# Kernel optimization log

Measured on AMD Instinct MI355X. Metric: run time of the kernel, lower is better.

The kernel has to match this reference:

```python
import jax, jax.numpy as jnp
import numpy as np

B, S, D, N = 8, 4096, 768, 64


def setup_inputs() -> dict:
    key = jax.random.key(0)
    k1, k2 = jax.random.split(key)
    word_vectors = jax.random.normal(k1, (B, S, D), dtype=jnp.float32)
    sent_rep_token_ids = jnp.sort(jax.random.randint(k2, (B, N), 0, S), axis=1)
    sent_rep_mask = jnp.ones((B, N), dtype=jnp.float32)
    # sent_lengths: each row must sum exactly to S (torch.split contract).
    rng = np.random.default_rng(0)
    lens = np.stack([
        np.diff(np.concatenate([[0], np.sort(rng.choice(np.arange(1, S), N - 1, replace=False)), [S]]))
        for _ in range(B)
    ])
    sent_lengths = jnp.asarray(lens, dtype=jnp.int64) if jax.config.jax_enable_x64 else jnp.asarray(lens, dtype=jnp.int32)
    sent_lengths_mask = jnp.ones((B, N), dtype=jnp.float32)
    return {
        "word_vectors": word_vectors,
        "sent_rep_token_ids": sent_rep_token_ids,
        "sent_rep_mask": sent_rep_mask,
        "sent_lengths": sent_lengths,
        "sent_lengths_mask": sent_lengths_mask,
    }


def reference(word_vectors, sent_rep_token_ids, sent_rep_mask, sent_lengths, sent_lengths_mask):
    b, s, d = word_vectors.shape
    n = sent_lengths.shape[1]
    dt = word_vectors.dtype

    # --- sent_rep_tokens branch: gather CLS-style token per sentence ---
    rep_vec = jnp.take_along_axis(word_vectors, sent_rep_token_ids[:, :, None], axis=1)  # [B,N,D]
    rep_vec = rep_vec * sent_rep_mask[:, :, None].astype(dt)

    # --- mean_tokens branch: ragged per-segment mean via segment_sum ---
    ends = jnp.cumsum(sent_lengths, axis=1)                      # [B,N] exclusive-end offsets
    pos = jnp.arange(s)
    seg = jax.vmap(lambda e: jnp.searchsorted(e, pos, side='right'))(ends)  # [B,S] segment id per token
    gseg = (seg + jnp.arange(b)[:, None] * n).reshape(-1)        # global segment ids [B*S]
    flat = word_vectors.reshape(b * s, d)
    sums = jax.ops.segment_sum(flat, gseg, num_segments=b * n).reshape(b, n, d)
    counts = jax.ops.segment_sum((flat != 0).astype(dt), gseg, num_segments=b * n).reshape(b, n, d)
    mean = sums / jnp.maximum(counts, 1)
    # fallback to word_vectors[0,0] when a segment has zero nonzero entries (original semantics)
    all_zero = (counts.sum(axis=-1) == 0)                        # [B,N]
    mean = jnp.where(all_zero[:, :, None], word_vectors[0, 0], mean)
    mean_vec = mean * sent_lengths_mask[:, :, None].astype(dt)

    out_vectors = jnp.concatenate([rep_vec, mean_vec], axis=1)   # [B,2N,D]
    out_masks = jnp.concatenate([sent_rep_mask, sent_lengths_mask], axis=1)  # [B,2N]
    return out_vectors, out_masks
```

## Files before the change

### kernel.cpp

```cpp
#include <hip/hip_runtime.h>

#define BB 8
#define SS 4096
#define DD 768
#define NN 64
#define D4 (DD / 4)

__global__ __launch_bounds__(64) void pool_kernel(
    const float* __restrict__ wv,
    const int* __restrict__ rep_ids,
    const float* __restrict__ rep_mask,
    const int* __restrict__ lens,
    const float* __restrict__ len_mask,
    float* __restrict__ out)
{
    const int seg  = blockIdx.x;
    const int g    = blockIdx.y;
    const int b    = seg >> 6;
    const int n    = seg & 63;
    const int lane = threadIdx.x;

    int myLen = lens[b * NN + lane];
    int pre   = (lane < n) ? myLen : 0;
    #pragma unroll
    for (int off = 32; off; off >>= 1) pre += __shfl_xor(pre, off);
    const int start = pre;
    const int len   = __shfl(myLen, n);

    const int col4 = g * 64 + lane;
    const float4* wv4 = (const float4*)wv;
    const float4* p   = wv4 + (size_t)(b * SS + start) * D4 + col4;

    float4 sum = make_float4(0.f, 0.f, 0.f, 0.f);
    float4 cnt = make_float4(0.f, 0.f, 0.f, 0.f);
    #pragma unroll 4
    for (int t = 0; t < len; ++t) {
        float4 v = p[(size_t)t * D4];
        sum.x += v.x; sum.y += v.y; sum.z += v.z; sum.w += v.w;
        cnt.x += (v.x != 0.f) ? 1.f : 0.f;
        cnt.y += (v.y != 0.f) ? 1.f : 0.f;
        cnt.z += (v.z != 0.f) ? 1.f : 0.f;
        cnt.w += (v.w != 0.f) ? 1.f : 0.f;
    }

    float4 mean;
    mean.x = sum.x / fmaxf(cnt.x, 1.f);
    mean.y = sum.y / fmaxf(cnt.y, 1.f);
    mean.z = sum.z / fmaxf(cnt.z, 1.f);
    mean.w = sum.w / fmaxf(cnt.w, 1.f);

    float tot = cnt.x + cnt.y + cnt.z + cnt.w;
    unsigned long long nz = __ballot(tot != 0.f);
    if (nz == 0ULL) {
        mean = wv4[col4];
    }

    const float lm = len_mask[b * NN + n];
    mean.x *= lm; mean.y *= lm; mean.z *= lm; mean.w *= lm;

    float4* out4 = (float4*)out;
    out4[(size_t)(b * 2 * NN + NN + n) * D4 + col4] = mean;

    const int   rid = rep_ids[b * NN + n];
    const float rm  = rep_mask[b * NN + n];
    float4 rv = wv4[(size_t)(b * SS + rid) * D4 + col4];
    rv.x *= rm; rv.y *= rm; rv.z *= rm; rv.w *= rm;
    out4[(size_t)(b * 2 * NN + n) * D4 + col4] = rv;

    if (g == 0 && lane == 0) {
        float* masks = out + (size_t)BB * 2 * NN * DD;
        masks[b * 2 * NN + n]      = rm;
        masks[b * 2 * NN + NN + n] = lm;
    }
}

extern "C" void kernel_launch(void* const* d_in, const int* in_sizes, int n_in,
                              void* d_out, int out_size, void* d_ws, size_t ws_size,
                              hipStream_t stream) {
    const float* wv       = (const float*)d_in[0];
    const int*   rep_ids  = (const int*)d_in[1];
    const float* rep_mask = (const float*)d_in[2];
    const int*   lens     = (const int*)d_in[3];
    const float* len_mask = (const float*)d_in[4];
    float*       out      = (float*)d_out;

    dim3 grid(BB * NN, 3);
    pool_kernel<<<grid, 64, 0, stream>>>(wv, rep_ids, rep_mask, lens, len_mask, out);
}
```

Baseline: 195.2 us.

## Split each segment's token loop across eight waves with shared-memory reduction

Each block now runs eight wavefronts. Each wave accumulates a strided subset of the segment's tokens, then wave 0 reduces the partial sums and counts held in LDS and writes the outputs. Before, a single wave walked the whole ragged segment serially, which gave only 1536 waves in flight and long per-wave dependency chains on a bandwidth-bound read of about 100 MB. The change adds a __syncthreads and an LDS reduction, and it leaves seven waves idle during the epilogue.

```diff
diff --git a/kernel.cpp b/kernel.cpp
--- a/kernel.cpp
+++ b/kernel.cpp
@@ -5,8 +5,10 @@
 #define DD 768
 #define NN 64
 #define D4 (DD / 4)
+#define WAVES 8
+#define BLOCK (WAVES * 64)
 
-__global__ __launch_bounds__(64) void pool_kernel(
+__global__ __launch_bounds__(BLOCK) void pool_kernel(
     const float* __restrict__ wv,
     const int* __restrict__ rep_ids,
     const float* __restrict__ rep_mask,
@@ -14,11 +16,16 @@
     const float* __restrict__ len_mask,
     float* __restrict__ out)
 {
+    __shared__ float4 s_sum[WAVES][64];
+    __shared__ float4 s_cnt[WAVES][64];
+
     const int seg  = blockIdx.x;
     const int g    = blockIdx.y;
     const int b    = seg >> 6;
     const int n    = seg & 63;
-    const int lane = threadIdx.x;
+    const int tid  = threadIdx.x;
+    const int lane = tid & 63;
+    const int w    = tid >> 6;
 
     int myLen = lens[b * NN + lane];
     int pre   = (lane < n) ? myLen : 0;
@@ -29,13 +36,14 @@
 
     const int col4 = g * 64 + lane;
     const float4* wv4 = (const float4*)wv;
-    const float4* p   = wv4 + (size_t)(b * SS + start) * D4 + col4;
+    const float4* p   = wv4 + ((size_t)(b * SS + start) + w) * D4 + col4;
 
     float4 sum = make_float4(0.f, 0.f, 0.f, 0.f);
     float4 cnt = make_float4(0.f, 0.f, 0.f, 0.f);
-    #pragma unroll 4
-    for (int t = 0; t < len; ++t) {
-        float4 v = p[(size_t)t * D4];
+    #pragma unroll 8
+    for (int t = w; t < len; t += WAVES) {
+        float4 v = *p;
+        p += (size_t)WAVES * D4;
         sum.x += v.x; sum.y += v.y; sum.z += v.z; sum.w += v.w;
         cnt.x += (v.x != 0.f) ? 1.f : 0.f;
         cnt.y += (v.y != 0.f) ? 1.f : 0.f;
@@ -43,34 +51,50 @@
         cnt.w += (v.w != 0.f) ? 1.f : 0.f;
     }
 
-    float4 mean;
-    mean.x = sum.x / fmaxf(cnt.x, 1.f);
-    mean.y = sum.y / fmaxf(cnt.y, 1.f);
-    mean.z = sum.z / fmaxf(cnt.z, 1.f);
-    mean.w = sum.w / fmaxf(cnt.w, 1.f);
+    s_sum[w][lane] = sum;
+    s_cnt[w][lane] = cnt;
+    __syncthreads();
 
-    float tot = cnt.x + cnt.y + cnt.z + cnt.w;
-    unsigned long long nz = __ballot(tot != 0.f);
-    if (nz == 0ULL) {
-        mean = wv4[col4];
-    }
+    if (w == 0) {
+        float4 S = make_float4(0.f, 0.f, 0.f, 0.f);
+        float4 C = make_float4(0.f, 0.f, 0.f, 0.f);
+        #pragma unroll
+        for (int j = 0; j < WAVES; ++j) {
+            float4 a = s_sum[j][lane];
+            float4 c = s_cnt[j][lane];
+            S.x += a.x; S.y += a.y; S.z += a.z; S.w += a.w;
+            C.x += c.x; C.y += c.y; C.z += c.z; C.w += c.w;
+        }
 
-    const float lm = len_mask[b * NN + n];
-    mean.x *= lm; mean.y *= lm; mean.z *= lm; mean.w *= lm;
+        float4 mean;
+        mean.x = S.x / fmaxf(C.x, 1.f);
+        mean.y = S.y / fmaxf(C.y, 1.f);
+        mean.z = S.z / fmaxf(C.z, 1.f);
+        mean.w = S.w / fmaxf(C.w, 1.f);
 
-    float4* out4 = (float4*)out;
-    out4[(size_t)(b * 2 * NN + NN + n) * D4 + col4] = mean;
+        float tot = C.x + C.y + C.z + C.w;
+        unsigned long long nz = __ballot(tot != 0.f);
+        if (nz == 0ULL) {
+            mean = wv4[col4];
+        }
 
-    const int   rid = rep_ids[b * NN + n];
-    const float rm  = rep_mask[b * NN + n];
-    float4 rv = wv4[(size_t)(b * SS + rid) * D4 + col4];
-    rv.x *= rm; rv.y *= rm; rv.z *= rm; rv.w *= rm;
-    out4[(size_t)(b * 2 * NN + n) * D4 + col4] = rv;
+        const float lm = len_mask[b * NN + n];
+        mean.x *= lm; mean.y *= lm; mean.z *= lm; mean.w *= lm;
 
-    if (g == 0 && lane == 0) {
-        float* masks = out + (size_t)BB * 2 * NN * DD;
-        masks[b * 2 * NN + n]      = rm;
-        masks[b * 2 * NN + NN + n] = lm;
+        float4* out4 = (float4*)out;
+        out4[(size_t)(b * 2 * NN + NN + n) * D4 + col4] = mean;
+
+        const int   rid = rep_ids[b * NN + n];
+        const float rm  = rep_mask[b * NN + n];
+        float4 rv = wv4[(size_t)(b * SS + rid) * D4 + col4];
+        rv.x *= rm; rv.y *= rm; rv.z *= rm; rv.w *= rm;
+        out4[(size_t)(b * 2 * NN + n) * D4 + col4] = rv;
+
+        if (g == 0 && lane == 0) {
+            float* masks = out + (size_t)BB * 2 * NN * DD;
+            masks[b * 2 * NN + n]      = rm;
+            masks[b * 2 * NN + NN + n] = lm;
+        }
     }
 }
 
@@ -85,5 +109,5 @@
     float*       out      = (float*)d_out;
 
     dim3 grid(BB * NN, 3);
-    pool_kernel<<<grid, 64, 0, stream>>>(wv, rep_ids, rep_mask, lens, len_mask, out);
+    pool_kernel<<<grid, BLOCK, 0, stream>>>(wv, rep_ids, rep_mask, lens, len_mask, out);
 }
```

New measurement: 159.0 us. -18.5%, faster.
